# Performance work log

Measured on AMD Instinct MI355X. Metric: run time of the kernel, lower is better.

The kernel has to match this reference:

```python
import jax, jax.numpy as jnp
import numpy as np

IOU_THRESHOLD = 0.5
EPS = 1e-7


def _make_boxes(key, n, h, w):
    k1, k2, k3, k4 = jax.random.split(key, 4)
    x1 = jax.random.uniform(k1, (n,)) * (w - 120.0)
    y1 = jax.random.uniform(k2, (n,)) * (h - 120.0)
    x2 = x1 + 20.0 + jax.random.uniform(k3, (n,)) * 100.0
    y2 = y1 + 20.0 + jax.random.uniform(k4, (n,)) * 100.0
    return jnp.stack([x1, y1, x2, y2], axis=1).astype(jnp.float32)


def setup_inputs() -> dict:
    key = jax.random.key(0)
    kd, ka, km, kt = jax.random.split(key, 4)
    N, K, H, W, MH, MW = 512, 100, 800, 800, 28, 28
    detections = _make_boxes(kd, N, H, W)[None]          # (1, N, 4) pixel coords
    annotations = _make_boxes(ka, K, H, W)[None]          # (1, K, 4) pixel coords
    masks = jax.random.uniform(km, (1, N, MH, MW, K), dtype=jnp.float32)
    masks_target = jax.random.uniform(kt, (1, K, H, W), dtype=jnp.float32)
    return {"detections": detections, "masks": masks,
            "annotations": annotations, "masks_target": masks_target}


def _overlap(a, b):
    # a: (N,4), b: (K,4) -> IoU (N,K)
    area = (b[:, 2] - b[:, 0]) * (b[:, 3] - b[:, 1])                      # (K,)
    iw = jnp.minimum(a[:, 2:3], b[None, :, 2]) - jnp.maximum(a[:, 0:1], b[None, :, 0])
    ih = jnp.minimum(a[:, 3:4], b[None, :, 3]) - jnp.maximum(a[:, 1:2], b[None, :, 1])
    iw = jnp.maximum(iw, 0.0)
    ih = jnp.maximum(ih, 0.0)
    inter = iw * ih
    ua = ((a[:, 2] - a[:, 0]) * (a[:, 3] - a[:, 1]))[:, None] + area[None, :] - inter
    return inter / jnp.maximum(ua, EPS)


def _crop_and_resize(images, boxes, box_ind, crop_size):
    # TF crop_and_resize (bilinear, extrapolation_value=0) on single-channel images.
    # images: (B, H, W); boxes: (M,4) normalized [y1,x1,y2,x2]; box_ind: (M,) int
    H, W = images.shape[1], images.shape[2]
    ch, cw = crop_size
    y1, x1, y2, x2 = boxes[:, 0], boxes[:, 1], boxes[:, 2], boxes[:, 3]
    gy = jnp.arange(ch, dtype=boxes.dtype) / (ch - 1)
    gx = jnp.arange(cw, dtype=boxes.dtype) / (cw - 1)
    in_y = (y1[:, None] + (y2 - y1)[:, None] * gy) * (H - 1)  # (M, ch)
    in_x = (x1[:, None] + (x2 - x1)[:, None] * gx) * (W - 1)  # (M, cw)
    valid_y = (in_y >= 0) & (in_y <= H - 1)
    valid_x = (in_x >= 0) & (in_x <= W - 1)
    y0 = jnp.floor(in_y)
    x0 = jnp.floor(in_x)
    yf = (in_y - y0)[:, :, None]
    xf = (in_x - x0)[:, None, :]
    y0i = jnp.clip(y0.astype(jnp.int32), 0, H - 1)
    y1i = jnp.clip(y0i + 1, 0, H - 1)
    x0i = jnp.clip(x0.astype(jnp.int32), 0, W - 1)
    x1i = jnp.clip(x0i + 1, 0, W - 1)
    b = box_ind[:, None, None]
    v00 = images[b, y0i[:, :, None], x0i[:, None, :]]
    v01 = images[b, y0i[:, :, None], x1i[:, None, :]]
    v10 = images[b, y1i[:, :, None], x0i[:, None, :]]
    v11 = images[b, y1i[:, :, None], x1i[:, None, :]]
    top = v00 + (v01 - v00) * xf
    bot = v10 + (v11 - v10) * xf
    out = top + (bot - top) * yf                                # (M, ch, cw)
    return jnp.where(valid_y[:, :, None] & valid_x[:, None, :], out, 0.0)


def reference(detections, masks, annotations, masks_target):
    d = detections[0]          # (N, 4)
    m = masks[0]               # (N, mh, mw, C)
    a = annotations[0]         # (K, 4)
    mt = masks_target[0]       # (K, H, W)
    N, mh, mw = m.shape[0], m.shape[1], m.shape[2]
    H, W = mt.shape[1], mt.shape[2]

    iou = _overlap(d, a)                               # (N, K)
    argmax_inds = jnp.argmax(iou, axis=1)              # (N,)
    max_iou = jnp.max(iou, axis=1)                     # (N,)
    valid = (max_iou >= IOU_THRESHOLD).astype(d.dtype)  # mask instead of dynamic gather

    x1, y1, x2, y2 = d[:, 0], d[:, 1], d[:, 2], d[:, 3]
    boxes = jnp.stack([y1 / H, x1 / W, y2 / H, x2 / W], axis=1)  # (N,4) normalized

    target = _crop_and_resize(mt, boxes, argmax_inds, (mh, mw))  # (N, mh, mw)
    # select the mask channel matching the assigned annotation index
    m_sel = jnp.take_along_axis(m, argmax_inds[:, None, None, None], axis=3)[..., 0]

    diff = jnp.abs(m_sel - target) * valid[:, None, None]
    n_sel = jnp.sum(valid)
    divisor = jnp.maximum(n_sel * mh * mw, 1.0)
    return jnp.sum(diff) / divisor
```

## Files before the change

### kernel.cpp

```cpp
#include <hip/hip_runtime.h>
#include <math.h>

#define N_DET 512
#define K_ANN 100
#define MH    28
#define MW    28
#define NPIX  (MH * MW)
#define IMH   800
#define IMW   800
#define BLOCKS_PER_DET 3
#define IOU_THRESH 0.5f
#define EPS_F 1e-7f


__global__ __launch_bounds__(128) void iou_argmax(
    const float* __restrict__ det,
    const float* __restrict__ ann,
    int* __restrict__ wsi)
{
    __shared__ float sv[128];
    __shared__ int   si[128];

    const int n   = blockIdx.x;
    const int tid = threadIdx.x;

    const float dx1 = det[n * 4 + 0];
    const float dy1 = det[n * 4 + 1];
    const float dx2 = det[n * 4 + 2];
    const float dy2 = det[n * 4 + 3];

    float best = -1.0f;
    int   bidx = 0x7FFFFFFF;
    if (tid < K_ANN) {
        const float ax1 = ann[tid * 4 + 0];
        const float ay1 = ann[tid * 4 + 1];
        const float ax2 = ann[tid * 4 + 2];
        const float ay2 = ann[tid * 4 + 3];
        const float area_k = (ax2 - ax1) * (ay2 - ay1);
        float iw = fminf(dx2, ax2) - fmaxf(dx1, ax1);
        float ih = fminf(dy2, ay2) - fmaxf(dy1, ay1);
        iw = fmaxf(iw, 0.0f);
        ih = fmaxf(ih, 0.0f);
        const float inter = iw * ih;
        const float ua = (dx2 - dx1) * (dy2 - dy1) + area_k - inter;
        best = inter / fmaxf(ua, EPS_F);
        bidx = tid;
    }

    sv[tid] = best;
    si[tid] = bidx;
    __syncthreads();
    for (int s = 64; s > 0; s >>= 1) {
        if (tid < s) {
            const float ov = sv[tid + s];
            const int   oi = si[tid + s];
            if (ov > sv[tid] || (ov == sv[tid] && oi < si[tid])) {
                sv[tid] = ov;
                si[tid] = oi;
            }
        }
        __syncthreads();
    }

    if (tid == 0 && sv[0] >= IOU_THRESH) {
        const int pos = atomicAdd(&wsi[0], 1);
        wsi[2 + pos] = (n << 7) | si[0];
    }
}

__global__ __launch_bounds__(256) void pixel_loss(
    const float* __restrict__ det,
    const float* __restrict__ masks,
    const float* __restrict__ mt,
    const int*   __restrict__ wsi,
    float*       __restrict__ wsf)
{
    const int b   = blockIdx.x;
    const int idx = b / BLOCKS_PER_DET;
    const int rem = b - idx * BLOCKS_PER_DET;

    const int count = wsi[0];
    if (idx >= count) return;

    const int packed = wsi[2 + idx];
    const int n = packed >> 7;
    const int k = packed & 127;

    const float dx1 = det[n * 4 + 0];
    const float dy1 = det[n * 4 + 1];
    const float dx2 = det[n * 4 + 2];
    const float dy2 = det[n * 4 + 3];

    const float by1 = dy1 / (float)IMH;
    const float bx1 = dx1 / (float)IMW;
    const float by2 = dy2 / (float)IMH;
    const float bx2 = dx2 / (float)IMW;

    const float* __restrict__ img = mt + (size_t)k * (IMH * IMW);
    const float* __restrict__ msk = masks + (size_t)n * NPIX * K_ANN + k;

    float local = 0.0f;
    for (int p = rem * 256 + threadIdx.x; p < NPIX; p += BLOCKS_PER_DET * 256) {
        const int i = p / MW;
        const int j = p - i * MW;
        const float gy = (float)i * (1.0f / (float)(MH - 1));
        const float gx = (float)j * (1.0f / (float)(MW - 1));
        const float in_y = (by1 + (by2 - by1) * gy) * (float)(IMH - 1);
        const float in_x = (bx1 + (bx2 - bx1) * gx) * (float)(IMW - 1);
        const bool vy = (in_y >= 0.0f) && (in_y <= (float)(IMH - 1));
        const bool vx = (in_x >= 0.0f) && (in_x <= (float)(IMW - 1));
        const float y0f = floorf(in_y);
        const float x0f = floorf(in_x);
        const float yf = in_y - y0f;
        const float xf = in_x - x0f;
        int y0i = (int)y0f;
        int x0i = (int)x0f;
        y0i = min(max(y0i, 0), IMH - 1);
        x0i = min(max(x0i, 0), IMW - 1);
        const int y1i = min(y0i + 1, IMH - 1);
        const int x1i = min(x0i + 1, IMW - 1);

        const float v00 = img[y0i * IMW + x0i];
        const float v01 = img[y0i * IMW + x1i];
        const float v10 = img[y1i * IMW + x0i];
        const float v11 = img[y1i * IMW + x1i];
        const float top = v00 + (v01 - v00) * xf;
        const float bot = v10 + (v11 - v10) * xf;
        float outv = top + (bot - top) * yf;
        outv = (vy && vx) ? outv : 0.0f;

        const float msel = msk[(size_t)p * K_ANN];
        local += fabsf(msel - outv);
    }

    for (int off = 32; off > 0; off >>= 1)
        local += __shfl_down(local, off);

    __shared__ float wsum[4];
    const int wave = threadIdx.x >> 6;
    const int lane = threadIdx.x & 63;
    if (lane == 0) wsum[wave] = local;
    __syncthreads();
    if (threadIdx.x == 0)
        atomicAdd(&wsf[1], (wsum[0] + wsum[1]) + (wsum[2] + wsum[3]));
}

__global__ void maskloss_final(const int* __restrict__ wsi,
                               const float* __restrict__ wsf,
                               float* __restrict__ out)
{
    const float c = (float)wsi[0];
    const float divisor = fmaxf(c * (float)NPIX, 1.0f);
    out[0] = wsf[1] / divisor;
}

extern "C" void kernel_launch(void* const* d_in, const int* in_sizes, int n_in,
                              void* d_out, int out_size, void* d_ws, size_t ws_size,
                              hipStream_t stream) {
    const float* det   = (const float*)d_in[0];
    const float* masks = (const float*)d_in[1];
    const float* ann   = (const float*)d_in[2];
    const float* mt    = (const float*)d_in[3];
    float* out = (float*)d_out;
    int*   wsi = (int*)d_ws;
    float* wsf = (float*)d_ws;

    hipMemsetAsync(d_ws, 0, 2 * sizeof(float), stream);

    iou_argmax<<<N_DET, 128, 0, stream>>>(det, ann, wsi);
    pixel_loss<<<N_DET * BLOCKS_PER_DET, 256, 0, stream>>>(det, masks, mt, wsi, wsf);
    maskloss_final<<<1, 1, 0, stream>>>(wsi, wsf, out);
}
```

Before: 350.5 us.

## Fuse IoU argmax, pixel loss and finalize into one kernel with last-block reduction

The three kernels (IoU argmax, per-pixel bilinear loss, final divide) are merged into a single launch with one block per detection. The argmax now runs in one wave using shuffles, and the finishing step is handled by whichever block increments a completion counter last. This removes two kernel launches and the compacted index list between stages. In exchange each block does all 784 pixels with 256 threads instead of spreading them over three blocks, and the finish relies on a threadfence plus atomic counter.

```diff
diff --git a/kernel.cpp b/kernel.cpp
--- a/kernel.cpp
+++ b/kernel.cpp
@@ -8,18 +8,22 @@
 #define NPIX  (MH * MW)
 #define IMH   800
 #define IMW   800
-#define BLOCKS_PER_DET 3
 #define IOU_THRESH 0.5f
 #define EPS_F 1e-7f
 
 
-__global__ __launch_bounds__(128) void iou_argmax(
+__global__ __launch_bounds__(256) void maskloss_fused(
     const float* __restrict__ det,
+    const float* __restrict__ masks,
     const float* __restrict__ ann,
-    int* __restrict__ wsi)
+    const float* __restrict__ mt,
+    int*   __restrict__ wsi,
+    float* __restrict__ wsf,
+    float* __restrict__ out)
 {
-    __shared__ float sv[128];
-    __shared__ int   si[128];
+    __shared__ float s_iou;
+    __shared__ int   s_k;
+    __shared__ float wsum[4];
 
     const int n   = blockIdx.x;
     const int tid = threadIdx.x;
@@ -29,129 +33,101 @@
     const float dx2 = det[n * 4 + 2];
     const float dy2 = det[n * 4 + 3];
 
-    float best = -1.0f;
-    int   bidx = 0x7FFFFFFF;
-    if (tid < K_ANN) {
-        const float ax1 = ann[tid * 4 + 0];
-        const float ay1 = ann[tid * 4 + 1];
-        const float ax2 = ann[tid * 4 + 2];
-        const float ay2 = ann[tid * 4 + 3];
-        const float area_k = (ax2 - ax1) * (ay2 - ay1);
-        float iw = fminf(dx2, ax2) - fmaxf(dx1, ax1);
-        float ih = fminf(dy2, ay2) - fmaxf(dy1, ay1);
-        iw = fmaxf(iw, 0.0f);
-        ih = fmaxf(ih, 0.0f);
-        const float inter = iw * ih;
-        const float ua = (dx2 - dx1) * (dy2 - dy1) + area_k - inter;
-        best = inter / fmaxf(ua, EPS_F);
-        bidx = tid;
+    if (tid < 64) {
+        const float darea = (dx2 - dx1) * (dy2 - dy1);
+        float best = -1.0f;
+        int   bidx = 0x7FFFFFFF;
+        for (int k = tid; k < K_ANN; k += 64) {
+            const float ax1 = ann[k * 4 + 0];
+            const float ay1 = ann[k * 4 + 1];
+            const float ax2 = ann[k * 4 + 2];
+            const float ay2 = ann[k * 4 + 3];
+            const float area_k = (ax2 - ax1) * (ay2 - ay1);
+            float iw = fminf(dx2, ax2) - fmaxf(dx1, ax1);
+            float ih = fminf(dy2, ay2) - fmaxf(dy1, ay1);
+            iw = fmaxf(iw, 0.0f);
+            ih = fmaxf(ih, 0.0f);
+            const float inter = iw * ih;
+            const float ua = darea + area_k - inter;
+            const float iou = inter / fmaxf(ua, EPS_F);
+            if (iou > best) { best = iou; bidx = k; }
+        }
+        for (int m = 32; m > 0; m >>= 1) {
+            const float ov = __shfl_xor(best, m);
+            const int   oi = __shfl_xor(bidx, m);
+            if (ov > best || (ov == best && oi < bidx)) { best = ov; bidx = oi; }
+        }
+        if (tid == 0) { s_iou = best; s_k = bidx; }
+    }
+    __syncthreads();
+
+    const bool valid = (s_iou >= IOU_THRESH);
+    const int  k     = s_k;
+
+    if (valid) {
+        const float by1 = dy1 / (float)IMH;
+        const float bx1 = dx1 / (float)IMW;
+        const float by2 = dy2 / (float)IMH;
+        const float bx2 = dx2 / (float)IMW;
+
+        const float* __restrict__ img = mt    + (size_t)k * (IMH * IMW);
+        const float* __restrict__ msk = masks + (size_t)n * (NPIX * K_ANN) + k;
+
+        auto px = [&](int p) -> float {
+            const int i = p / MW;
+            const int j = p - i * MW;
+            const float gy = (float)i * (1.0f / (float)(MH - 1));
+            const float gx = (float)j * (1.0f / (float)(MW - 1));
+            const float in_y = (by1 + (by2 - by1) * gy) * (float)(IMH - 1);
+            const float in_x = (bx1 + (bx2 - bx1) * gx) * (float)(IMW - 1);
+            const bool vy = (in_y >= 0.0f) && (in_y <= (float)(IMH - 1));
+            const bool vx = (in_x >= 0.0f) && (in_x <= (float)(IMW - 1));
+            const float y0f = floorf(in_y);
+            const float x0f = floorf(in_x);
+            const float yf = in_y - y0f;
+            const float xf = in_x - x0f;
+            int y0i = (int)y0f;
+            int x0i = (int)x0f;
+            y0i = min(max(y0i, 0), IMH - 1);
+            x0i = min(max(x0i, 0), IMW - 1);
+            const int y1i = min(y0i + 1, IMH - 1);
+            const int x1i = min(x0i + 1, IMW - 1);
+
+            const float msel = msk[(size_t)p * K_ANN];
+            const float v00 = img[y0i * IMW + x0i];
+            const float v01 = img[y0i * IMW + x1i];
+            const float v10 = img[y1i * IMW + x0i];
+            const float v11 = img[y1i * IMW + x1i];
+            const float top = v00 + (v01 - v00) * xf;
+            const float bot = v10 + (v11 - v10) * xf;
+            float outv = top + (bot - top) * yf;
+            outv = (vy && vx) ? outv : 0.0f;
+            return fabsf(msel - outv);
+        };
+
+        float local = px(tid) + px(tid + 256) + px(tid + 512);
+        if (tid < 16) local += px(tid + 768);
+
+        for (int off = 32; off > 0; off >>= 1)
+            local += __shfl_down(local, off);
+        const int wave = tid >> 6;
+        const int lane = tid & 63;
+        if (lane == 0) wsum[wave] = local;
+        __syncthreads();
+        if (tid == 0) {
+            atomicAdd(&wsf[1], (wsum[0] + wsum[1]) + (wsum[2] + wsum[3]));
+            atomicAdd(&wsi[0], 1);
+        }
     }
 
-    sv[tid] = best;
-    si[tid] = bidx;
-    __syncthreads();
-    for (int s = 64; s > 0; s >>= 1) {
-        if (tid < s) {
-            const float ov = sv[tid + s];
-            const int   oi = si[tid + s];
-            if (ov > sv[tid] || (ov == sv[tid] && oi < si[tid])) {
-                sv[tid] = ov;
-                si[tid] = oi;
-            }
+    __threadfence();
+    if (tid == 0) {
+        if (atomicAdd(&wsi[2], 1) == N_DET - 1) {
+            const int   c = atomicAdd(&wsi[0], 0);
+            const float s = atomicAdd(&wsf[1], 0.0f);
+            out[0] = s / fmaxf((float)c * (float)NPIX, 1.0f);
         }
-        __syncthreads();
     }
-
-    if (tid == 0 && sv[0] >= IOU_THRESH) {
-        const int pos = atomicAdd(&wsi[0], 1);
-        wsi[2 + pos] = (n << 7) | si[0];
-    }
-}
-
-__global__ __launch_bounds__(256) void pixel_loss(
-    const float* __restrict__ det,
-    const float* __restrict__ masks,
-    const float* __restrict__ mt,
-    const int*   __restrict__ wsi,
-    float*       __restrict__ wsf)
-{
-    const int b   = blockIdx.x;
-    const int idx = b / BLOCKS_PER_DET;
-    const int rem = b - idx * BLOCKS_PER_DET;
-
-    const int count = wsi[0];
-    if (idx >= count) return;
-
-    const int packed = wsi[2 + idx];
-    const int n = packed >> 7;
-    const int k = packed & 127;
-
-    const float dx1 = det[n * 4 + 0];
-    const float dy1 = det[n * 4 + 1];
-    const float dx2 = det[n * 4 + 2];
-    const float dy2 = det[n * 4 + 3];
-
-    const float by1 = dy1 / (float)IMH;
-    const float bx1 = dx1 / (float)IMW;
-    const float by2 = dy2 / (float)IMH;
-    const float bx2 = dx2 / (float)IMW;
-
-    const float* __restrict__ img = mt + (size_t)k * (IMH * IMW);
-    const float* __restrict__ msk = masks + (size_t)n * NPIX * K_ANN + k;
-
-    float local = 0.0f;
-    for (int p = rem * 256 + threadIdx.x; p < NPIX; p += BLOCKS_PER_DET * 256) {
-        const int i = p / MW;
-        const int j = p - i * MW;
-        const float gy = (float)i * (1.0f / (float)(MH - 1));
-        const float gx = (float)j * (1.0f / (float)(MW - 1));
-        const float in_y = (by1 + (by2 - by1) * gy) * (float)(IMH - 1);
-        const float in_x = (bx1 + (bx2 - bx1) * gx) * (float)(IMW - 1);
-        const bool vy = (in_y >= 0.0f) && (in_y <= (float)(IMH - 1));
-        const bool vx = (in_x >= 0.0f) && (in_x <= (float)(IMW - 1));
-        const float y0f = floorf(in_y);
-        const float x0f = floorf(in_x);
-        const float yf = in_y - y0f;
-        const float xf = in_x - x0f;
-        int y0i = (int)y0f;
-        int x0i = (int)x0f;
-        y0i = min(max(y0i, 0), IMH - 1);
-        x0i = min(max(x0i, 0), IMW - 1);
-        const int y1i = min(y0i + 1, IMH - 1);
-        const int x1i = min(x0i + 1, IMW - 1);
-
-        const float v00 = img[y0i * IMW + x0i];
-        const float v01 = img[y0i * IMW + x1i];
-        const float v10 = img[y1i * IMW + x0i];
-        const float v11 = img[y1i * IMW + x1i];
-        const float top = v00 + (v01 - v00) * xf;
-        const float bot = v10 + (v11 - v10) * xf;
-        float outv = top + (bot - top) * yf;
-        outv = (vy && vx) ? outv : 0.0f;
-
-        const float msel = msk[(size_t)p * K_ANN];
-        local += fabsf(msel - outv);
-    }
-
-    for (int off = 32; off > 0; off >>= 1)
-        local += __shfl_down(local, off);
-
-    __shared__ float wsum[4];
-    const int wave = threadIdx.x >> 6;
-    const int lane = threadIdx.x & 63;
-    if (lane == 0) wsum[wave] = local;
-    __syncthreads();
-    if (threadIdx.x == 0)
-        atomicAdd(&wsf[1], (wsum[0] + wsum[1]) + (wsum[2] + wsum[3]));
-}
-
-__global__ void maskloss_final(const int* __restrict__ wsi,
-                               const float* __restrict__ wsf,
-                               float* __restrict__ out)
-{
-    const float c = (float)wsi[0];
-    const float divisor = fmaxf(c * (float)NPIX, 1.0f);
-    out[0] = wsf[1] / divisor;
 }
 
 extern "C" void kernel_launch(void* const* d_in, const int* in_sizes, int n_in,
@@ -165,9 +141,7 @@
     int*   wsi = (int*)d_ws;
     float* wsf = (float*)d_ws;
 
-    hipMemsetAsync(d_ws, 0, 2 * sizeof(float), stream);
+    hipMemsetAsync(d_ws, 0, 3 * sizeof(int), stream);
 
-    iou_argmax<<<N_DET, 128, 0, stream>>>(det, ann, wsi);
-    pixel_loss<<<N_DET * BLOCKS_PER_DET, 256, 0, stream>>>(det, masks, mt, wsi, wsf);
-    maskloss_final<<<1, 1, 0, stream>>>(wsi, wsf, out);
+    maskloss_fused<<<N_DET, 256, 0, stream>>>(det, masks, ann, mt, wsi, wsf, out);
 }
```

New measurement: 403.5 us. 15.1% more time.
